# Kernel optimization log

Measured on AMD Instinct MI355X. Metric: run time of the kernel, lower is better.

## Reference

```python
import jax, jax.numpy as jnp
import numpy as np

TEMP = 0.07
BASE_TEMP = 0.07
EPS = 1e-8


def setup_inputs() -> dict:
    key = jax.random.key(0)
    features = jax.random.normal(key, (4096, 2, 128), dtype=jnp.float32)
    return {"features": features}


def reference(features):
    B, V, D = features.shape  # bsz, n_views, dim
    # torch.cat(torch.unbind(features, dim=1), dim=0): view-major ordering
    cf = jnp.swapaxes(features, 0, 1).reshape(V * B, D)  # [N, D], N = V*B
    # cosine similarity = normalize rows then GEMM (same math as broadcasted CosineSimilarity)
    n = cf / jnp.maximum(jnp.linalg.norm(cf, axis=-1, keepdims=True), EPS)
    logits = jnp.matmul(n, n.T) / TEMP  # [N, N]
    N = V * B
    logits_mask = 1.0 - jnp.eye(N, dtype=logits.dtype)  # zero out self-contrast
    # SimCLR mask: eye(B) tiled over (anchor_count, contrast_count), minus diagonal
    pos_mask = jnp.tile(jnp.eye(B, dtype=logits.dtype), (V, V)) * logits_mask
    exp_logits = jnp.exp(logits) * logits_mask
    log_prob = logits - jnp.log(exp_logits.sum(axis=1, keepdims=True))
    mean_log_prob_pos = (pos_mask * log_prob).sum(axis=1) / pos_mask.sum(axis=1)
    loss = -(TEMP / BASE_TEMP) * mean_log_prob_pos
    return loss.reshape(V, B).mean()
```

## Files before the change

kernel.cpp:

```cpp
#include <hip/hip_runtime.h>
#include <hip/hip_bf16.h>
#include <math.h>


constexpr int   Bsz   = 4096;
constexpr int   Nrows = 8192;
constexpr int   Dd    = 128;
constexpr float TEMPf = 0.07f;
constexpr float EPSN  = 1e-8f;
constexpr float SCALE = 1.4426950408889634f / 0.07f;
constexpr float LN2   = 0.6931471805599453f;

constexpr int CHUNKS     = 32;
constexpr int CHUNK_COLS = Nrows / CHUNKS;
constexpr int TILES      = CHUNK_COLS / 32;
constexpr int ROWS_BLK   = 256;
constexpr int NPAIRS     = CHUNKS * (CHUNKS + 1) / 2;
constexpr int YG         = Nrows / ROWS_BLK;
constexpr int PREPBLKS   = Bsz / 4;

typedef __attribute__((ext_vector_type(8)))  short bf16x8;
typedef __attribute__((ext_vector_type(16))) float floatx16;


constexpr size_t OFF_PART = 0x200000;
constexpr size_t OFF_SPOS = 0x300000;

__device__ __forceinline__ void gld_lds16(const void* g, void* l) {
    __builtin_amdgcn_global_load_lds(
        (const __attribute__((address_space(1))) void*)g,
        (__attribute__((address_space(3))) void*)l, 16, 0, 0);
}

__global__ void prep_k(const float* __restrict__ f,
                       char* __restrict__ nF,
                       float* __restrict__ sposPart,
                       float* __restrict__ out) {
    __shared__ float sred[4];
    int tid  = threadIdx.x;
    int wid  = tid >> 6;
    int lane = tid & 63;
    int b    = blockIdx.x * 4 + wid;
    if (blockIdx.x == 0 && tid == 0) out[0] = 0.f;

    const float* s0 = f + (size_t)(b * 2) * Dd;
    float2 x = *(const float2*)(s0 + lane * 2);
    float2 y = *(const float2*)(s0 + Dd + lane * 2);
    float ss0 = x.x * x.x + x.y * x.y;
    float ss1 = y.x * y.x + y.y * y.y;
    float dt  = x.x * y.x + x.y * y.y;
    #pragma unroll
    for (int off = 32; off; off >>= 1) {
        ss0 += __shfl_xor(ss0, off);
        ss1 += __shfl_xor(ss1, off);
        dt  += __shfl_xor(dt,  off);
    }
    float inv0 = 1.0f / fmaxf(sqrtf(ss0), EPSN);
    float inv1 = 1.0f / fmaxf(sqrtf(ss1), EPSN);

    size_t poff = (size_t)(lane >> 3) * 1024 + ((lane >> 2) & 1) * 512
                + (lane & 3) * 4;

    __hip_bfloat162 h;
    h.x = __float2bfloat16(x.x * inv0);
    h.y = __float2bfloat16(x.y * inv0);
    *(__hip_bfloat162*)(nF + (size_t)(b >> 5) * 8192 + (b & 31) * 16 + poff) = h;
    int r1 = Bsz + b;
    h.x = __float2bfloat16(y.x * inv1);
    h.y = __float2bfloat16(y.y * inv1);
    *(__hip_bfloat162*)(nF + (size_t)(r1 >> 5) * 8192 + (r1 & 31) * 16 + poff) = h;

    if (lane == 0) sred[wid] = dt * inv0 * inv1 / TEMPf;
    __syncthreads();
    if (tid == 0) sposPart[blockIdx.x] = sred[0] + sred[1] + sred[2] + sred[3];
}

__global__ __launch_bounds__(256, 3)
void main_k(const char* __restrict__ nF, float* __restrict__ partial) {
    __shared__ char  bufs[2][8192];
    __shared__ float colred[4][256];
    __shared__ float rred[256];
    const int tid  = threadIdx.x;
    const int wid  = tid >> 6;
    const int lane = tid & 63;
    const int lo   = lane & 31;
    const int hi   = lane >> 5;

    int p = blockIdx.x, ci = 0;
    while (p >= CHUNKS - ci) { p -= CHUNKS - ci; ci++; }
    const int cj = ci + p;

    const int rbase = ci * ROWS_BLK + wid * 64;
    const int cbase = cj * ROWS_BLK;
    const int cg0   = cj * 8;

    bf16x8 afrag[2][8];
    #pragma unroll
    for (int s = 0; s < 2; s++) {
        const char* ag = nF + (size_t)((rbase + s * 32) >> 5) * 8192 + lane * 16;
        #pragma unroll
        for (int kc = 0; kc < 8; kc++)
            afrag[s][kc] = *(const bf16x8*)(ag + kc * 1024);
    }

    float rs[2][16];
    #pragma unroll
    for (int s = 0; s < 2; s++)
        #pragma unroll
        for (int r = 0; r < 16; r++) rs[s][r] = 0.f;

    {
        const char* g0 = nF + (size_t)cg0 * 8192;
        int kc = wid * 2;
        gld_lds16(g0 + kc * 1024 + lane * 16,       &bufs[0][kc * 1024]);
        gld_lds16(g0 + (kc + 1) * 1024 + lane * 16, &bufs[0][(kc + 1) * 1024]);
    }

    #pragma unroll 1
    for (int t = 0; t < TILES; t++) {
        __syncthreads();
        if (t + 1 < TILES) {
            const char* gn = nF + (size_t)(cg0 + t + 1) * 8192;
            char* dst = bufs[(t + 1) & 1];
            int kc = wid * 2;
            gld_lds16(gn + kc * 1024 + lane * 16,       dst + kc * 1024);
            gld_lds16(gn + (kc + 1) * 1024 + lane * 16, dst + (kc + 1) * 1024);
        }

        const char* buf = bufs[t & 1];
        floatx16 acc0 = {}, acc1 = {};
        #pragma unroll
        for (int kc = 0; kc < 8; kc++) {
            bf16x8 bf = *(const bf16x8*)&buf[kc * 1024 + lane * 16];
            acc0 = __builtin_amdgcn_mfma_f32_32x32x16_bf16(afrag[0][kc], bf, acc0, 0, 0, 0);
            acc1 = __builtin_amdgcn_mfma_f32_32x32x16_bf16(afrag[1][kc], bf, acc1, 0, 0, 0);
        }

        const int cb32 = cbase + t * 32;
        float cs = 0.f;
        #pragma unroll
        for (int s = 0; s < 2; s++) {
            const floatx16& acc = s ? acc1 : acc0;
            if (cb32 == rbase + s * 32) {
                #pragma unroll
                for (int r = 0; r < 16; r++) {
                    float e = __builtin_amdgcn_exp2f(acc[r] * SCALE);
                    if (lo == ((r & 3) + 8 * (r >> 2) + 4 * hi)) e = 0.f;
                    cs += e; rs[s][r] += e;
                }
            } else {
                #pragma unroll
                for (int r = 0; r < 16; r++) {
                    float e = __builtin_amdgcn_exp2f(acc[r] * SCALE);
                    cs += e; rs[s][r] += e;
                }
            }
        }
        cs += __shfl_xor(cs, 32);
        if (hi == 0) colred[wid][t * 32 + lo] = cs;
    }

    if (ci != cj) {
        #pragma unroll
        for (int s = 0; s < 2; s++) {
            #pragma unroll
            for (int r = 0; r < 16; r++) {
                float v = rs[s][r];
                v += __shfl_xor(v, 1);
                v += __shfl_xor(v, 2);
                v += __shfl_xor(v, 4);
                v += __shfl_xor(v, 8);
                v += __shfl_xor(v, 16);
                if (lo == r)
                    rred[wid * 64 + s * 32 + ((r & 3) + 8 * (r >> 2) + 4 * hi)] = v;
            }
        }
    }

    __syncthreads();
    float v = colred[0][tid] + colred[1][tid] + colred[2][tid] + colred[3][tid];
    partial[(size_t)ci * Nrows + cbase + tid] = v;
    if (ci != cj)
        partial[(size_t)cj * Nrows + ci * ROWS_BLK + tid] = rred[tid];
}

__global__ __launch_bounds__(256)
void final_k(const float* __restrict__ partial, const float* __restrict__ sposPart,
             float* __restrict__ out) {
    __shared__ float red[4];
    int tid = threadIdx.x;
    int r = blockIdx.x * 256 + tid;
    float se = 0.f;
    #pragma unroll
    for (int p = 0; p < YG; p++) se += partial[(size_t)p * Nrows + r];
    float acc = __builtin_amdgcn_logf(se) * LN2;
    if (tid < 32) acc -= 2.f * sposPart[blockIdx.x * 32 + tid];
    #pragma unroll
    for (int off = 32; off; off >>= 1) acc += __shfl_xor(acc, off);
    if ((tid & 63) == 0) red[tid >> 6] = acc;
    __syncthreads();
    if (tid == 0)
        atomicAdd(out, (red[0] + red[1] + red[2] + red[3]) / (float)Nrows);
}

extern "C" void kernel_launch(void* const* d_in, const int* in_sizes, int n_in,
                              void* d_out, int out_size, void* d_ws, size_t ws_size,
                              hipStream_t stream) {
    const float* f = (const float*)d_in[0];
    char* ws = (char*)d_ws;
    char* nF        = ws;
    float* partial  = (float*)(ws + OFF_PART);
    float* sposPart = (float*)(ws + OFF_SPOS);

    prep_k<<<PREPBLKS, 256, 0, stream>>>(f, nF, sposPart, (float*)d_out);
    main_k<<<NPAIRS, 256, 0, stream>>>(nF, partial);
    final_k<<<Nrows / 256, 256, 0, stream>>>(partial, sposPart, (float*)d_out);
}
```

Measured before the change: 81.15 us.

## Triple-buffer LDS tile staging with explicit vmcnt waits and unrolled loop

```diff
diff --git a/kernel.cpp b/kernel.cpp
--- a/kernel.cpp
+++ b/kernel.cpp
@@ -77,7 +77,7 @@
 
 __global__ __launch_bounds__(256, 3)
 void main_k(const char* __restrict__ nF, float* __restrict__ partial) {
-    __shared__ char  bufs[2][8192];
+    __shared__ char  bufs[3][8192];
     __shared__ float colred[4][256];
     __shared__ float rred[256];
     const int tid  = threadIdx.x;
@@ -109,25 +109,15 @@
         #pragma unroll
         for (int r = 0; r < 16; r++) rs[s][r] = 0.f;
 
-    {
-        const char* g0 = nF + (size_t)cg0 * 8192;
+    auto stage = [&](int bi, int cg) {
+        const char* g = nF + (size_t)cg * 8192;
         int kc = wid * 2;
-        gld_lds16(g0 + kc * 1024 + lane * 16,       &bufs[0][kc * 1024]);
-        gld_lds16(g0 + (kc + 1) * 1024 + lane * 16, &bufs[0][(kc + 1) * 1024]);
-    }
-
-    #pragma unroll 1
-    for (int t = 0; t < TILES; t++) {
-        __syncthreads();
-        if (t + 1 < TILES) {
-            const char* gn = nF + (size_t)(cg0 + t + 1) * 8192;
-            char* dst = bufs[(t + 1) & 1];
-            int kc = wid * 2;
-            gld_lds16(gn + kc * 1024 + lane * 16,       dst + kc * 1024);
-            gld_lds16(gn + (kc + 1) * 1024 + lane * 16, dst + (kc + 1) * 1024);
-        }
-
-        const char* buf = bufs[t & 1];
+        gld_lds16(g + kc * 1024 + lane * 16,       &bufs[bi][kc * 1024]);
+        gld_lds16(g + (kc + 1) * 1024 + lane * 16, &bufs[bi][(kc + 1) * 1024]);
+    };
+
+    auto compute = [&](int bi, int t) {
+        const char* buf = bufs[bi];
         floatx16 acc0 = {}, acc1 = {};
         #pragma unroll
         for (int kc = 0; kc < 8; kc++) {
@@ -135,7 +125,6 @@
             acc0 = __builtin_amdgcn_mfma_f32_32x32x16_bf16(afrag[0][kc], bf, acc0, 0, 0, 0);
             acc1 = __builtin_amdgcn_mfma_f32_32x32x16_bf16(afrag[1][kc], bf, acc1, 0, 0, 0);
         }
-
         const int cb32 = cbase + t * 32;
         float cs = 0.f;
         #pragma unroll
@@ -158,6 +147,19 @@
         }
         cs += __shfl_xor(cs, 32);
         if (hi == 0) colred[wid][t * 32 + lo] = cs;
+    };
+
+    stage(0, cg0 + 0);
+    stage(1, cg0 + 1);
+
+    #pragma unroll
+    for (int t = 0; t < TILES; t++) {
+        if (t < TILES - 1)
+            asm volatile("s_waitcnt vmcnt(2)\n\ts_barrier" ::: "memory");
+        else
+            asm volatile("s_waitcnt vmcnt(0)\n\ts_barrier" ::: "memory");
+        if (t + 2 < TILES) stage((t + 2) % 3, cg0 + t + 2);
+        compute(t % 3, t);
     }
 
     if (ci != cj) {
```

New measurement: 123.6 us. 1.52x slower.

## Fuse prep, main, and final kernels into one cooperative kernel with grid syncs

Applied to the files above, without the earlier changes.

```diff
diff --git a/kernel.cpp b/kernel.cpp
--- a/kernel.cpp
+++ b/kernel.cpp
@@ -1,6 +1,9 @@
 #include <hip/hip_runtime.h>
 #include <hip/hip_bf16.h>
+#include <hip/hip_cooperative_groups.h>
 #include <math.h>
+
+namespace cg = cooperative_groups;
 
 
 constexpr int   Bsz   = 4096;
@@ -18,6 +21,7 @@
 constexpr int NPAIRS     = CHUNKS * (CHUNKS + 1) / 2;
 constexpr int YG         = Nrows / ROWS_BLK;
 constexpr int PREPBLKS   = Bsz / 4;
+constexpr int PREPWAVES  = NPAIRS * 4;
 
 typedef __attribute__((ext_vector_type(8)))  short bf16x8;
 typedef __attribute__((ext_vector_type(16))) float floatx16;
@@ -30,6 +34,190 @@
     __builtin_amdgcn_global_load_lds(
         (const __attribute__((address_space(1))) void*)g,
         (__attribute__((address_space(3))) void*)l, 16, 0, 0);
+}
+
+__device__ __forceinline__ float prep_row(const float* __restrict__ f,
+                                          char* __restrict__ nF,
+                                          int b, int lane) {
+    const float* s0 = f + (size_t)(b * 2) * Dd;
+    float2 x = *(const float2*)(s0 + lane * 2);
+    float2 y = *(const float2*)(s0 + Dd + lane * 2);
+    float ss0 = x.x * x.x + x.y * x.y;
+    float ss1 = y.x * y.x + y.y * y.y;
+    float dt  = x.x * y.x + x.y * y.y;
+    #pragma unroll
+    for (int off = 32; off; off >>= 1) {
+        ss0 += __shfl_xor(ss0, off);
+        ss1 += __shfl_xor(ss1, off);
+        dt  += __shfl_xor(dt,  off);
+    }
+    float inv0 = 1.0f / fmaxf(sqrtf(ss0), EPSN);
+    float inv1 = 1.0f / fmaxf(sqrtf(ss1), EPSN);
+
+    size_t poff = (size_t)(lane >> 3) * 1024 + ((lane >> 2) & 1) * 512
+                + (lane & 3) * 4;
+
+    __hip_bfloat162 h;
+    h.x = __float2bfloat16(x.x * inv0);
+    h.y = __float2bfloat16(x.y * inv0);
+    *(__hip_bfloat162*)(nF + (size_t)(b >> 5) * 8192 + (b & 31) * 16 + poff) = h;
+    int r1 = Bsz + b;
+    h.x = __float2bfloat16(y.x * inv1);
+    h.y = __float2bfloat16(y.y * inv1);
+    *(__hip_bfloat162*)(nF + (size_t)(r1 >> 5) * 8192 + (r1 & 31) * 16 + poff) = h;
+
+    return dt * inv0 * inv1 / TEMPf;
+}
+
+__global__ __launch_bounds__(256, 3)
+void fused_k(const float* __restrict__ f, char* __restrict__ nF,
+             float* __restrict__ partial, float* __restrict__ sposPart,
+             float* __restrict__ out) {
+    __shared__ char  bufs[2][8192];
+    __shared__ float colred[4][256];
+    __shared__ float rred[256];
+    __shared__ float sredP[4];
+    const int tid  = threadIdx.x;
+    const int wid  = tid >> 6;
+    const int lane = tid & 63;
+    const int lo   = lane & 31;
+    const int hi   = lane >> 5;
+
+    if (blockIdx.x == 0 && tid == 0) out[0] = 0.f;
+    {
+        int wgid = blockIdx.x * 4 + wid;
+        float sdt = 0.f;
+        for (int b = wgid; b < Bsz; b += PREPWAVES)
+            sdt += prep_row(f, nF, b, lane);
+        if (lane == 0) sredP[wid] = sdt;
+    }
+    __syncthreads();
+    if (tid == 0) sposPart[blockIdx.x] = sredP[0] + sredP[1] + sredP[2] + sredP[3];
+    __threadfence();
+    cg::this_grid().sync();
+
+    int p = blockIdx.x, ci = 0;
+    while (p >= CHUNKS - ci) { p -= CHUNKS - ci; ci++; }
+    const int cj = ci + p;
+
+    const int rbase = ci * ROWS_BLK + wid * 64;
+    const int cbase = cj * ROWS_BLK;
+    const int cg0   = cj * 8;
+
+    bf16x8 afrag[2][8];
+    #pragma unroll
+    for (int g = 0; g < 2; g++) {
+        const char* ag = nF + (size_t)((rbase + g * 32) >> 5) * 8192 + lane * 16;
+        #pragma unroll
+        for (int kc = 0; kc < 8; kc++)
+            afrag[g][kc] = *(const bf16x8*)(ag + kc * 1024);
+    }
+
+    float rs[2][16];
+    #pragma unroll
+    for (int g = 0; g < 2; g++)
+        #pragma unroll
+        for (int r = 0; r < 16; r++) rs[g][r] = 0.f;
+
+    {
+        const char* g0 = nF + (size_t)cg0 * 8192;
+        int kc = wid * 2;
+        gld_lds16(g0 + kc * 1024 + lane * 16,       &bufs[0][kc * 1024]);
+        gld_lds16(g0 + (kc + 1) * 1024 + lane * 16, &bufs[0][(kc + 1) * 1024]);
+    }
+
+    #pragma unroll 1
+    for (int t = 0; t < TILES; t++) {
+        __syncthreads();
+        if (t + 1 < TILES) {
+            const char* gn = nF + (size_t)(cg0 + t + 1) * 8192;
+            char* dst = bufs[(t + 1) & 1];
+            int kc = wid * 2;
+            gld_lds16(gn + kc * 1024 + lane * 16,       dst + kc * 1024);
+            gld_lds16(gn + (kc + 1) * 1024 + lane * 16, dst + (kc + 1) * 1024);
+        }
+
+        const char* buf = bufs[t & 1];
+        floatx16 acc0 = {}, acc1 = {};
+        #pragma unroll
+        for (int kc = 0; kc < 8; kc++) {
+            bf16x8 bf = *(const bf16x8*)&buf[kc * 1024 + lane * 16];
+            acc0 = __builtin_amdgcn_mfma_f32_32x32x16_bf16(afrag[0][kc], bf, acc0, 0, 0, 0);
+            acc1 = __builtin_amdgcn_mfma_f32_32x32x16_bf16(afrag[1][kc], bf, acc1, 0, 0, 0);
+        }
+
+        const int cb32 = cbase + t * 32;
+        float cs = 0.f;
+        #pragma unroll
+        for (int g = 0; g < 2; g++) {
+            const floatx16& acc = g ? acc1 : acc0;
+            if (cb32 == rbase + g * 32) {
+                #pragma unroll
+                for (int r = 0; r < 16; r++) {
+                    float e = __builtin_amdgcn_exp2f(acc[r] * SCALE);
+                    if (lo == ((r & 3) + 8 * (r >> 2) + 4 * hi)) e = 0.f;
+                    cs += e; rs[g][r] += e;
+                }
+            } else {
+                #pragma unroll
+                for (int r = 0; r < 16; r++) {
+                    float e = __builtin_amdgcn_exp2f(acc[r] * SCALE);
+                    cs += e; rs[g][r] += e;
+                }
+            }
+        }
+        cs += __shfl_xor(cs, 32);
+        if (hi == 0) colred[wid][t * 32 + lo] = cs;
+    }
+
+    if (ci != cj) {
+        #pragma unroll
+        for (int g = 0; g < 2; g++) {
+            #pragma unroll
+            for (int r = 0; r < 16; r++) {
+                float v = rs[g][r];
+                v += __shfl_xor(v, 1);
+                v += __shfl_xor(v, 2);
+                v += __shfl_xor(v, 4);
+                v += __shfl_xor(v, 8);
+                v += __shfl_xor(v, 16);
+                if (lo == r)
+                    rred[wid * 64 + g * 32 + ((r & 3) + 8 * (r >> 2) + 4 * hi)] = v;
+            }
+        }
+    }
+
+    __syncthreads();
+    float v = colred[0][tid] + colred[1][tid] + colred[2][tid] + colred[3][tid];
+    partial[(size_t)ci * Nrows + cbase + tid] = v;
+    if (ci != cj)
+        partial[(size_t)cj * Nrows + ci * ROWS_BLK + tid] = rred[tid];
+
+    __threadfence();
+    cg::this_grid().sync();
+
+    if (blockIdx.x < YG) {
+        int r = blockIdx.x * 256 + tid;
+        float se = 0.f;
+        #pragma unroll
+        for (int q = 0; q < YG; q++) se += partial[(size_t)q * Nrows + r];
+        float acc = __builtin_amdgcn_logf(se) * LN2;
+        #pragma unroll
+        for (int off = 32; off; off >>= 1) acc += __shfl_xor(acc, off);
+        if ((tid & 63) == 0) rred[(tid >> 6)] = acc;
+        __syncthreads();
+        if (tid == 0)
+            atomicAdd(out, (rred[0] + rred[1] + rred[2] + rred[3]) / (float)Nrows);
+    } else if (blockIdx.x == YG) {
+        float s = sposPart[tid] + sposPart[tid + 256]
+                + (tid < NPAIRS - 512 ? sposPart[tid + 512] : 0.f);
+        #pragma unroll
+        for (int off = 32; off; off >>= 1) s += __shfl_xor(s, off);
+        if ((tid & 63) == 0) rred[(tid >> 6)] = s;
+        __syncthreads();
+        if (tid == 0)
+            atomicAdd(out, -2.f * (rred[0] + rred[1] + rred[2] + rred[3]) / (float)Nrows);
+    }
 }
 
 __global__ void prep_k(const float* __restrict__ f,
@@ -42,35 +230,8 @@
     int lane = tid & 63;
     int b    = blockIdx.x * 4 + wid;
     if (blockIdx.x == 0 && tid == 0) out[0] = 0.f;
-
-    const float* s0 = f + (size_t)(b * 2) * Dd;
-    float2 x = *(const float2*)(s0 + lane * 2);
-    float2 y = *(const float2*)(s0 + Dd + lane * 2);
-    float ss0 = x.x * x.x + x.y * x.y;
-    float ss1 = y.x * y.x + y.y * y.y;
-    float dt  = x.x * y.x + x.y * y.y;
-    #pragma unroll
-    for (int off = 32; off; off >>= 1) {
-        ss0 += __shfl_xor(ss0, off);
-        ss1 += __shfl_xor(ss1, off);
-        dt  += __shfl_xor(dt,  off);
-    }
-    float inv0 = 1.0f / fmaxf(sqrtf(ss0), EPSN);
-    float inv1 = 1.0f / fmaxf(sqrtf(ss1), EPSN);
-
-    size_t poff = (size_t)(lane >> 3) * 1024 + ((lane >> 2) & 1) * 512
-                + (lane & 3) * 4;
-
-    __hip_bfloat162 h;
-    h.x = __float2bfloat16(x.x * inv0);
-    h.y = __float2bfloat16(x.y * inv0);
-    *(__hip_bfloat162*)(nF + (size_t)(b >> 5) * 8192 + (b & 31) * 16 + poff) = h;
-    int r1 = Bsz + b;
-    h.x = __float2bfloat16(y.x * inv1);
-    h.y = __float2bfloat16(y.y * inv1);
-    *(__hip_bfloat162*)(nF + (size_t)(r1 >> 5) * 8192 + (r1 & 31) * 16 + poff) = h;
-
-    if (lane == 0) sred[wid] = dt * inv0 * inv1 / TEMPf;
+    float sdt = prep_row(f, nF, b, lane);
+    if (lane == 0) sred[wid] = sdt;
     __syncthreads();
     if (tid == 0) sposPart[blockIdx.x] = sred[0] + sred[1] + sred[2] + sred[3];
 }
@@ -96,18 +257,18 @@
 
     bf16x8 afrag[2][8];
     #pragma unroll
-    for (int s = 0; s < 2; s++) {
-        const char* ag = nF + (size_t)((rbase + s * 32) >> 5) * 8192 + lane * 16;
+    for (int g = 0; g < 2; g++) {
+        const char* ag = nF + (size_t)((rbase + g * 32) >> 5) * 8192 + lane * 16;
         #pragma unroll
         for (int kc = 0; kc < 8; kc++)
-            afrag[s][kc] = *(const bf16x8*)(ag + kc * 1024);
+            afrag[g][kc] = *(const bf16x8*)(ag + kc * 1024);
     }
 
     float rs[2][16];
     #pragma unroll
-    for (int s = 0; s < 2; s++)
-        #pragma unroll
-        for (int r = 0; r < 16; r++) rs[s][r] = 0.f;
+    for (int g = 0; g < 2; g++)
+        #pragma unroll
+        for (int r = 0; r < 16; r++) rs[g][r] = 0.f;
 
     {
         const char* g0 = nF + (size_t)cg0 * 8192;
@@ -139,20 +300,20 @@
         const int cb32 = cbase + t * 32;
         float cs = 0.f;
         #pragma unroll
-        for (int s = 0; s < 2; s++) {
-            const floatx16& acc = s ? acc1 : acc0;
-            if (cb32 == rbase + s * 32) {
+        for (int g = 0; g < 2; g++) {
+            const floatx16& acc = g ? acc1 : acc0;
+            if (cb32 == rbase + g * 32) {
                 #pragma unroll
                 for (int r = 0; r < 16; r++) {
                     float e = __builtin_amdgcn_exp2f(acc[r] * SCALE);
                     if (lo == ((r & 3) + 8 * (r >> 2) + 4 * hi)) e = 0.f;
-                    cs += e; rs[s][r] += e;
+                    cs += e; rs[g][r] += e;
                 }
             } else {
                 #pragma unroll
                 for (int r = 0; r < 16; r++) {
                     float e = __builtin_amdgcn_exp2f(acc[r] * SCALE);
-                    cs += e; rs[s][r] += e;
+                    cs += e; rs[g][r] += e;
                 }
             }
         }
@@ -162,17 +323,17 @@
 
     if (ci != cj) {
         #pragma unroll
-        for (int s = 0; s < 2; s++) {
+        for (int g = 0; g < 2; g++) {
             #pragma unroll
             for (int r = 0; r < 16; r++) {
-                float v = rs[s][r];
+                float v = rs[g][r];
                 v += __shfl_xor(v, 1);
                 v += __shfl_xor(v, 2);
                 v += __shfl_xor(v, 4);
                 v += __shfl_xor(v, 8);
                 v += __shfl_xor(v, 16);
                 if (lo == r)
-                    rred[wid * 64 + s * 32 + ((r & 3) + 8 * (r >> 2) + 4 * hi)] = v;
+                    rred[wid * 64 + g * 32 + ((r & 3) + 8 * (r >> 2) + 4 * hi)] = v;
             }
         }
     }
@@ -208,11 +369,18 @@
                               hipStream_t stream) {
     const float* f = (const float*)d_in[0];
     char* ws = (char*)d_ws;
-    char* nF        = ws;
+    char*  nF       = ws;
     float* partial  = (float*)(ws + OFF_PART);
     float* sposPart = (float*)(ws + OFF_SPOS);
-
-    prep_k<<<PREPBLKS, 256, 0, stream>>>(f, nF, sposPart, (float*)d_out);
-    main_k<<<NPAIRS, 256, 0, stream>>>(nF, partial);
-    final_k<<<Nrows / 256, 256, 0, stream>>>(partial, sposPart, (float*)d_out);
-}
+    float* outp     = (float*)d_out;
+
+    void* args[] = {(void*)&f, (void*)&nF, (void*)&partial, (void*)&sposPart,
+                    (void*)&outp};
+    hipError_t err = hipLaunchCooperativeKernel(
+        (const void*)fused_k, dim3(NPAIRS), dim3(256), args, 0, stream);
+    if (err != hipSuccess) {
+        prep_k<<<PREPBLKS, 256, 0, stream>>>(f, nF, sposPart, outp);
+        main_k<<<NPAIRS, 256, 0, stream>>>(nF, partial);
+        final_k<<<Nrows / 256, 256, 0, stream>>>(partial, sposPart, outp);
+    }
+}
```

After: 257.4 us. 217% more time.
